# Optimization experiments

Hardware: AMD Instinct MI355X
Metric: run time of the kernel (lower is better)

Reference implementation:

```python
import jax, jax.numpy as jnp
import numpy as np
import math

D_MODEL = 2048
NUM_HEADS = 16
QUERY_GROUPS = 4
HEAD_DIM = D_MODEL // NUM_HEADS  # 128
B, T = 2, 2048


def setup_inputs() -> dict:
    key = jax.random.key(0)
    ks = jax.random.split(key, 9)
    s = 0.02
    return {
        "x": jax.random.normal(ks[0], (B, T, D_MODEL), dtype=jnp.float32),
        "Wq": jax.random.normal(ks[1], (D_MODEL, NUM_HEADS * HEAD_DIM), dtype=jnp.float32) * s,
        "bq": jnp.zeros((NUM_HEADS * HEAD_DIM,), dtype=jnp.float32),
        "Wk": jax.random.normal(ks[2], (D_MODEL, QUERY_GROUPS * HEAD_DIM), dtype=jnp.float32) * s,
        "bk": jnp.zeros((QUERY_GROUPS * HEAD_DIM,), dtype=jnp.float32),
        "Wv": jax.random.normal(ks[3], (D_MODEL, QUERY_GROUPS * HEAD_DIM), dtype=jnp.float32) * s,
        "bv": jnp.zeros((QUERY_GROUPS * HEAD_DIM,), dtype=jnp.float32),
        "Wo": jax.random.normal(ks[4], (D_MODEL, D_MODEL), dtype=jnp.float32) * s,
        "bo": jnp.zeros((D_MODEL,), dtype=jnp.float32),
    }


def reference(x, Wq, bq, Wk, bk, Wv, bv, Wo, bo):
    Bb, Tt, Dd = x.shape
    G, H, hd = QUERY_GROUPS, NUM_HEADS, HEAD_DIM
    m = H // G  # heads per group
    # projections
    q = (x @ Wq + bq).reshape(Bb, Tt, G, m, hd)   # [B,T,G,m,hd]
    k = (x @ Wk + bk).reshape(Bb, Tt, G, hd)      # [B,T,G,hd]
    v = (x @ Wv + bv).reshape(Bb, Tt, G, hd)
    # scores with native group broadcast (no explicit K/V expansion)
    scores = jnp.einsum('btgmd,bsgd->bgmts', q, k) / math.sqrt(hd)  # [B,G,m,T,T]
    p = jax.nn.softmax(scores, axis=-1)
    out = jnp.einsum('bgmts,bsgd->btgmd', p, v).reshape(Bb, Tt, Dd)
    # output projection (dropout is identity in eval / p=0)
    return out @ Wo + bo
```

## Files before the change

### kernel.cpp

```cpp
#include <hip/hip_runtime.h>

#define D_MODEL 2048
#define T_SEQ   2048
#define NBATCH  2
#define NH      16
#define NG      4
#define HD      128
#define NQKV    3072

typedef short bf16x8 __attribute__((ext_vector_type(8)));
typedef float f32x4  __attribute__((ext_vector_type(4)));
typedef short s16x4  __attribute__((ext_vector_type(4)));

__device__ __forceinline__ short f2bf(float f) {
  union { float f; unsigned u; } v; v.f = f;
  unsigned r = v.u + 0x7fffu + ((v.u >> 16) & 1u);
  return (short)(r >> 16);
}

__device__ __forceinline__ short f2bf_fast(float f) {
  union { float f; unsigned u; } v; v.f = f;
  return (short)((v.u + 0x8000u) >> 16);
}

__device__ __forceinline__ float bf2f(short s) {
  union { unsigned u; float f; } v; v.u = ((unsigned)(unsigned short)s) << 16;
  return v.f;
}

__device__ __forceinline__ float fast_exp2(float x) {
#if __has_builtin(__builtin_amdgcn_exp2f)
  return __builtin_amdgcn_exp2f(x);
#else
  return __expf(x * 0.6931471805599453f);
#endif
}

__device__ __forceinline__ void gload16(const void* g, void* l) {
  __builtin_amdgcn_global_load_lds(
      (const __attribute__((address_space(1))) void*)g,
      (__attribute__((address_space(3))) void*)l, 16, 0, 0);
}

__global__ __launch_bounds__(256) void convert_x_kernel(
    const float* __restrict__ x, short* __restrict__ o, int n) {
  int i = (blockIdx.x * 256 + threadIdx.x) * 4;
  if (i >= n) return;
  float4 v = *(const float4*)(x + i);
  s16x4 s;
  s[0] = f2bf(v.x); s[1] = f2bf(v.y); s[2] = f2bf(v.z); s[3] = f2bf(v.w);
  *(s16x4*)(o + i) = s;
}

__global__ __launch_bounds__(256) void wtrans_kernel(
    const float* __restrict__ W, short* __restrict__ dst,
    int K, int N, int rowOff, int dstStride) {
  __shared__ float t[32][33];
  int tx = threadIdx.x & 31, ty = threadIdx.x >> 5;
  int kb = blockIdx.x * 32, nb = blockIdx.y * 32;
#pragma unroll
  for (int i = 0; i < 4; ++i)
    t[ty + 8*i][tx] = W[(long)(kb + ty + 8*i) * N + nb + tx];
  __syncthreads();
#pragma unroll
  for (int i = 0; i < 4; ++i)
    dst[(long)(rowOff + nb + ty + 8*i) * dstStride + kb + tx] = f2bf(t[tx][ty + 8*i]);
}

__global__ __launch_bounds__(256) void vtrans_kernel(
    const short* __restrict__ qkv, short* __restrict__ vt) {
  __shared__ short t[32][33];
  int bg = blockIdx.z; int b = bg >> 2, g = bg & 3;
  int sb = blockIdx.x * 32, db = blockIdx.y * 32;
  int tx = threadIdx.x & 31, ty = threadIdx.x >> 5;
  const short* src = qkv + (long)(b * T_SEQ) * NQKV + D_MODEL + NG * HD + g * HD;
#pragma unroll
  for (int i = 0; i < 4; ++i)
    t[ty + 8*i][tx] = src[(long)(sb + ty + 8*i) * NQKV + db + tx];
  __syncthreads();
  short* dst = vt + ((long)bg * HD + db) * T_SEQ + sb;
#pragma unroll
  for (int i = 0; i < 4; ++i)
    dst[(long)(ty + 8*i) * T_SEQ + tx] = t[tx][ty + 8*i];
}

__global__ __launch_bounds__(256) void gemm_kernel(
    const short* __restrict__ A, const short* __restrict__ BT,
    const float* __restrict__ b0, const float* __restrict__ b1, const float* __restrict__ b2,
    void* __restrict__ Cout, int M, int N, int K, int mode) {
  __shared__ __align__(16) short As[128 * 64];
  __shared__ __align__(16) short Bs[128 * 64];
  const int tid = threadIdx.x;
  const int w = tid >> 6, lane = tid & 63;
  const int l15 = lane & 15, quad = lane >> 4;
  const int wr = w & 1, wc = w >> 1;
  const int nb = blockIdx.x, mb = blockIdx.y;
  const short* Ab = A + (long)mb * 128 * K;
  const short* Bb = BT + (long)nb * 128 * K;

  f32x4 acc[4][4];
#pragma unroll
  for (int i = 0; i < 4; ++i)
#pragma unroll
    for (int j = 0; j < 4; ++j) acc[i][j] = 0.0f;

  for (int k0 = 0; k0 < K; k0 += 64) {
    __syncthreads();
#pragma unroll
    for (int t = 0; t < 4; ++t) {
      int chunk = w * 256 + t * 64 + lane;
      int r = chunk >> 3, c = chunk & 7;
      int gc = c ^ (r & 7);
      gload16(Ab + (long)r * K + k0 + gc * 8, As + (w * 256 + t * 64) * 8);
      gload16(Bb + (long)r * K + k0 + gc * 8, Bs + (w * 256 + t * 64) * 8);
    }
    __syncthreads();
#pragma unroll
    for (int ks = 0; ks < 2; ++ks) {
      bf16x8 af[4], bfr[4];
#pragma unroll
      for (int i = 0; i < 4; ++i) {
        int r = wr * 64 + i * 16 + l15;
        af[i] = *(const bf16x8*)(As + r * 64 + (((ks * 4 + quad) ^ (r & 7)) * 8));
      }
#pragma unroll
      for (int j = 0; j < 4; ++j) {
        int r = wc * 64 + j * 16 + l15;
        bfr[j] = *(const bf16x8*)(Bs + r * 64 + (((ks * 4 + quad) ^ (r & 7)) * 8));
      }
#pragma unroll
      for (int i = 0; i < 4; ++i)
#pragma unroll
        for (int j = 0; j < 4; ++j)
          acc[i][j] = __builtin_amdgcn_mfma_f32_16x16x32_bf16(af[i], bfr[j], acc[i][j], 0, 0, 0);
    }
  }

  float biasv[4];
#pragma unroll
  for (int j = 0; j < 4; ++j) {
    int col = nb * 128 + wc * 64 + j * 16 + l15;
    float bv;
    if (mode == 0) {
      if (col < 2048)      bv = b0[col];
      else if (col < 2560) bv = b1[col - 2048];
      else                 bv = b2[col - 2560];
    } else bv = b0[col];
    biasv[j] = bv;
  }
  if (mode == 0) {
    short* C = (short*)Cout;
#pragma unroll
    for (int i = 0; i < 4; ++i)
#pragma unroll
      for (int j = 0; j < 4; ++j)
#pragma unroll
        for (int r = 0; r < 4; ++r) {
          int row = mb * 128 + wr * 64 + i * 16 + quad * 4 + r;
          int col = nb * 128 + wc * 64 + j * 16 + l15;
          C[(long)row * N + col] = f2bf(acc[i][j][r] + biasv[j]);
        }
  } else {
    float* C = (float*)Cout;
#pragma unroll
    for (int i = 0; i < 4; ++i)
#pragma unroll
      for (int j = 0; j < 4; ++j)
#pragma unroll
        for (int r = 0; r < 4; ++r) {
          int row = mb * 128 + wr * 64 + i * 16 + quad * 4 + r;
          int col = nb * 128 + wc * 64 + j * 16 + l15;
          C[(long)row * N + col] = acc[i][j][r] + biasv[j];
        }
  }
}

__global__ __launch_bounds__(256, 2) void attn_kernel(
    const short* __restrict__ qkv, const short* __restrict__ vt,
    short* __restrict__ aout) {
  __shared__ __align__(16) short smem[24576];
  short* Ks = smem;
  short* Vs = smem + 8192;
  short* Ps = smem + 16384;

  const int tid = threadIdx.x;
  const int w = tid >> 6, lane = tid & 63;
  const int l15 = lane & 15, quad = lane >> 4;
  const int qt = blockIdx.x, h = blockIdx.y, b = blockIdx.z;
  const int g = h >> 2;
  const short* qbase = qkv + (long)(b * T_SEQ + qt * 128) * NQKV + h * HD;
  const short* kbase = qkv + (long)(b * T_SEQ) * NQKV + D_MODEL + g * HD;
  const short* vbase = vt + (long)(b * NG + g) * HD * T_SEQ;
  const float QSCALE = 0.08838834764831845f * 1.4426950408889634f;

  int kroff[4], vroff[4], kdst[4], vdst[4];
#pragma unroll
  for (int t = 0; t < 4; ++t) {
    int chunk = w * 256 + t * 64 + lane;
    { int r = chunk >> 4, c = chunk & 15, gc = c ^ (r & 15);
      kroff[t] = r * NQKV + gc * 8; }
    { int r = chunk >> 3, c = chunk & 7, gc = c ^ (r & 7);
      vroff[t] = r * T_SEQ + gc * 8; }
    kdst[t] = chunk * 8; vdst[t] = chunk * 8;
  }

  bf16x8 qfrag[2][4];
#pragma unroll
  for (int set = 0; set < 2; ++set) {
    int qr = w * 32 + set * 16 + l15;
#pragma unroll
    for (int ks = 0; ks < 4; ++ks) {
      bf16x8 v = *(const bf16x8*)(qbase + (long)qr * NQKV + ks * 32 + quad * 8);
#pragma unroll
      for (int e = 0; e < 8; ++e) v[e] = f2bf(bf2f(v[e]) * QSCALE);
      qfrag[set][ks] = v;
    }
  }

#pragma unroll
  for (int t = 0; t < 4; ++t) {
    gload16(kbase + kroff[t], Ks + (w * 256 + t * 64) * 8);
    gload16(vbase + vroff[t], Vs + (w * 256 + t * 64) * 8);
  }

  bf16x8 ones;
#pragma unroll
  for (int e = 0; e < 8; ++e) ones[e] = (short)0x3F80;

  f32x4 lacc[2] = {f32x4(0.0f), f32x4(0.0f)};
  f32x4 oacc[2][8];
#pragma unroll
  for (int set = 0; set < 2; ++set)
#pragma unroll
    for (int j = 0; j < 8; ++j) oacc[set][j] = 0.0f;

  __syncthreads();

  bf16x8 kpre[4], vpre[4];
  for (int st = 0; st < T_SEQ / 64; ++st) {
    const bool pf = (st + 1 < T_SEQ / 64);
    if (pf) {
      const short* kb2 = kbase + (long)(st + 1) * 64 * NQKV;
      const short* vb2 = vbase + (st + 1) * 64;
#pragma unroll
      for (int t = 0; t < 4; ++t) {
        kpre[t] = *(const bf16x8*)(kb2 + kroff[t]);
        vpre[t] = *(const bf16x8*)(vb2 + vroff[t]);
      }
    }

    f32x4 sacc[2][4];
#pragma unroll
    for (int set = 0; set < 2; ++set)
#pragma unroll
      for (int j = 0; j < 4; ++j) sacc[set][j] = 0.0f;
    __builtin_amdgcn_s_setprio(1);
#pragma unroll
    for (int ks = 0; ks < 4; ++ks) {
#pragma unroll
      for (int j = 0; j < 4; ++j) {
        int krow = j * 16 + l15;
        bf16x8 bfr = *(const bf16x8*)(Ks + krow * 128 + (((ks * 4 + quad) ^ (krow & 15)) * 8));
        sacc[0][j] = __builtin_amdgcn_mfma_f32_16x16x32_bf16(qfrag[0][ks], bfr, sacc[0][j], 0, 0, 0);
        sacc[1][j] = __builtin_amdgcn_mfma_f32_16x16x32_bf16(qfrag[1][ks], bfr, sacc[1][j], 0, 0, 0);
      }
    }
    __builtin_amdgcn_s_setprio(0);

#pragma unroll
    for (int set = 0; set < 2; ++set)
#pragma unroll
      for (int j = 0; j < 4; ++j)
#pragma unroll
        for (int r = 0; r < 4; ++r) {
          short pb = f2bf_fast(fast_exp2(sacc[set][j][r]));
          int row = w * 32 + set * 16 + quad * 4 + r;
          int col = j * 16 + l15;
          Ps[row * 64 + (((col >> 3) ^ (row & 7)) * 8) + (col & 7)] = pb;
        }

    const int qr0 = w * 32 + l15, qr1 = qr0 + 16;
    __builtin_amdgcn_s_setprio(1);
#pragma unroll
    for (int ks = 0; ks < 2; ++ks) {
      bf16x8 af0 = *(const bf16x8*)(Ps + qr0 * 64 + (((ks * 4 + quad) ^ (qr0 & 7)) * 8));
      bf16x8 af1 = *(const bf16x8*)(Ps + qr1 * 64 + (((ks * 4 + quad) ^ (qr1 & 7)) * 8));
      lacc[0] = __builtin_amdgcn_mfma_f32_16x16x32_bf16(af0, ones, lacc[0], 0, 0, 0);
      lacc[1] = __builtin_amdgcn_mfma_f32_16x16x32_bf16(af1, ones, lacc[1], 0, 0, 0);
#pragma unroll
      for (int j = 0; j < 8; ++j) {
        int vrow = j * 16 + l15;
        bf16x8 bfr = *(const bf16x8*)(Vs + vrow * 64 + (((ks * 4 + quad) ^ (vrow & 7)) * 8));
        oacc[0][j] = __builtin_amdgcn_mfma_f32_16x16x32_bf16(af0, bfr, oacc[0][j], 0, 0, 0);
        oacc[1][j] = __builtin_amdgcn_mfma_f32_16x16x32_bf16(af1, bfr, oacc[1][j], 0, 0, 0);
      }
    }
    __builtin_amdgcn_s_setprio(0);

    __syncthreads();
    if (pf) {
#pragma unroll
      for (int t = 0; t < 4; ++t) {
        *(bf16x8*)(Ks + kdst[t]) = kpre[t];
        *(bf16x8*)(Vs + vdst[t]) = vpre[t];
      }
    }
    __syncthreads();
  }

  short* obase = aout + (long)(b * T_SEQ + qt * 128) * D_MODEL + h * HD;
#pragma unroll
  for (int set = 0; set < 2; ++set) {
    float inv[4];
#pragma unroll
    for (int r = 0; r < 4; ++r) inv[r] = 1.0f / lacc[set][r];
#pragma unroll
    for (int j = 0; j < 8; ++j)
#pragma unroll
      for (int r = 0; r < 4; ++r) {
        int row = w * 32 + set * 16 + quad * 4 + r;
        int col = j * 16 + l15;
        obase[(long)row * D_MODEL + col] = f2bf(oacc[set][j][r] * inv[r]);
      }
  }
}

extern "C" void kernel_launch(void* const* d_in, const int* in_sizes, int n_in,
                              void* d_out, int out_size, void* d_ws, size_t ws_size,
                              hipStream_t stream) {
  const float* x  = (const float*)d_in[0];
  const float* Wq = (const float*)d_in[1];
  const float* bq = (const float*)d_in[2];
  const float* Wk = (const float*)d_in[3];
  const float* bk = (const float*)d_in[4];
  const float* Wv = (const float*)d_in[5];
  const float* bv = (const float*)d_in[6];
  const float* Wo = (const float*)d_in[7];
  const float* bo = (const float*)d_in[8];

  const long NTOK = (long)NBATCH * T_SEQ;
  short* xb    = (short*)d_ws;
  short* wqkvT = xb + NTOK * D_MODEL;
  short* woT   = wqkvT + (long)NQKV * D_MODEL;
  short* qkvb  = woT + (long)D_MODEL * D_MODEL;
  short* vtb   = qkvb + NTOK * NQKV;
  short* attnb = vtb + (long)NBATCH * NG * HD * T_SEQ;

  int nX = (int)(NTOK * D_MODEL);
  convert_x_kernel<<<nX / (256 * 4), 256, 0, stream>>>(x, xb, nX);
  wtrans_kernel<<<dim3(D_MODEL / 32, D_MODEL / 32), 256, 0, stream>>>(Wq, wqkvT, D_MODEL, D_MODEL, 0, D_MODEL);
  wtrans_kernel<<<dim3(D_MODEL / 32, 512 / 32), 256, 0, stream>>>(Wk, wqkvT, D_MODEL, 512, 2048, D_MODEL);
  wtrans_kernel<<<dim3(D_MODEL / 32, 512 / 32), 256, 0, stream>>>(Wv, wqkvT, D_MODEL, 512, 2560, D_MODEL);
  wtrans_kernel<<<dim3(D_MODEL / 32, D_MODEL / 32), 256, 0, stream>>>(Wo, woT, D_MODEL, D_MODEL, 0, D_MODEL);

  gemm_kernel<<<dim3(NQKV / 128, NTOK / 128), 256, 0, stream>>>(
      xb, wqkvT, bq, bk, bv, (void*)qkvb, (int)NTOK, NQKV, D_MODEL, 0);

  vtrans_kernel<<<dim3(T_SEQ / 32, HD / 32, NBATCH * NG), 256, 0, stream>>>(qkvb, vtb);

  attn_kernel<<<dim3(T_SEQ / 128, NH, NBATCH), 256, 0, stream>>>(qkvb, vtb, attnb);

  gemm_kernel<<<dim3(D_MODEL / 128, NTOK / 128), 256, 0, stream>>>(
      attnb, woT, bo, bo, bo, (void*)d_out, (int)NTOK, D_MODEL, D_MODEL, 1);
}
```

Baseline: 330.9 us.

## Compute transposed attention with 32x32 MFMA, keep P in registers, stage output via LDS

Rewrites the attention inner loop to compute S^T = K·Q^T with 32x32x16 MFMAs, so each lane holds a query column's scores. The exponentiated scores are packed to bf16 with v_cvt_pk_bf16 and exchanged across half-waves with shuffles to form the P operand directly, removing the LDS round-trip for P and its extra LDS buffer. The row sum is accumulated in registers instead of via an MFMA against ones, and the output is staged through LDS so it can be written as coalesced 16-byte stores. The trade-off is more cross-lane shuffle and select work per tile and a higher register demand from the 16-wide accumulators.

```diff
diff --git a/kernel.cpp b/kernel.cpp
--- a/kernel.cpp
+++ b/kernel.cpp
@@ -10,17 +10,13 @@
 
 typedef short bf16x8 __attribute__((ext_vector_type(8)));
 typedef float f32x4  __attribute__((ext_vector_type(4)));
+typedef float f32x16 __attribute__((ext_vector_type(16)));
 typedef short s16x4  __attribute__((ext_vector_type(4)));
 
 __device__ __forceinline__ short f2bf(float f) {
   union { float f; unsigned u; } v; v.f = f;
   unsigned r = v.u + 0x7fffu + ((v.u >> 16) & 1u);
   return (short)(r >> 16);
-}
-
-__device__ __forceinline__ short f2bf_fast(float f) {
-  union { float f; unsigned u; } v; v.f = f;
-  return (short)((v.u + 0x8000u) >> 16);
 }
 
 __device__ __forceinline__ float bf2f(short s) {
@@ -34,6 +30,12 @@
 #else
   return __expf(x * 0.6931471805599453f);
 #endif
+}
+
+__device__ __forceinline__ unsigned cvt_pk_bf16(float a, float b) {
+  unsigned r;
+  asm("v_cvt_pk_bf16_f32 %0, %1, %2" : "=v"(r) : "v"(a), "v"(b));
+  return r;
 }
 
 __device__ __forceinline__ void gload16(const void* g, void* l) {
@@ -178,14 +180,13 @@
 __global__ __launch_bounds__(256, 2) void attn_kernel(
     const short* __restrict__ qkv, const short* __restrict__ vt,
     short* __restrict__ aout) {
-  __shared__ __align__(16) short smem[24576];
+  __shared__ __align__(16) short smem[16384];
   short* Ks = smem;
   short* Vs = smem + 8192;
-  short* Ps = smem + 16384;
 
   const int tid = threadIdx.x;
   const int w = tid >> 6, lane = tid & 63;
-  const int l15 = lane & 15, quad = lane >> 4;
+  const int l31 = lane & 31, hi = lane >> 5;
   const int qt = blockIdx.x, h = blockIdx.y, b = blockIdx.z;
   const int g = h >> 2;
   const short* qbase = qkv + (long)(b * T_SEQ + qt * 128) * NQKV + h * HD;
@@ -193,7 +194,7 @@
   const short* vbase = vt + (long)(b * NG + g) * HD * T_SEQ;
   const float QSCALE = 0.08838834764831845f * 1.4426950408889634f;
 
-  int kroff[4], vroff[4], kdst[4], vdst[4];
+  int kroff[4], vroff[4], dst[4];
 #pragma unroll
   for (int t = 0; t < 4; ++t) {
     int chunk = w * 256 + t * 64 + lane;
@@ -201,38 +202,31 @@
       kroff[t] = r * NQKV + gc * 8; }
     { int r = chunk >> 3, c = chunk & 7, gc = c ^ (r & 7);
       vroff[t] = r * T_SEQ + gc * 8; }
-    kdst[t] = chunk * 8; vdst[t] = chunk * 8;
-  }
-
-  bf16x8 qfrag[2][4];
-#pragma unroll
-  for (int set = 0; set < 2; ++set) {
-    int qr = w * 32 + set * 16 + l15;
-#pragma unroll
-    for (int ks = 0; ks < 4; ++ks) {
-      bf16x8 v = *(const bf16x8*)(qbase + (long)qr * NQKV + ks * 32 + quad * 8);
+    dst[t] = chunk * 8;
+  }
+
+  bf16x8 qfrag[8];
+  {
+    const short* qrow = qbase + (long)(w * 32 + l31) * NQKV + hi * 8;
+#pragma unroll
+    for (int ks = 0; ks < 8; ++ks) {
+      bf16x8 v = *(const bf16x8*)(qrow + ks * 16);
 #pragma unroll
       for (int e = 0; e < 8; ++e) v[e] = f2bf(bf2f(v[e]) * QSCALE);
-      qfrag[set][ks] = v;
+      qfrag[ks] = v;
     }
   }
 
 #pragma unroll
   for (int t = 0; t < 4; ++t) {
-    gload16(kbase + kroff[t], Ks + (w * 256 + t * 64) * 8);
-    gload16(vbase + vroff[t], Vs + (w * 256 + t * 64) * 8);
-  }
-
-  bf16x8 ones;
-#pragma unroll
-  for (int e = 0; e < 8; ++e) ones[e] = (short)0x3F80;
-
-  f32x4 lacc[2] = {f32x4(0.0f), f32x4(0.0f)};
-  f32x4 oacc[2][8];
-#pragma unroll
-  for (int set = 0; set < 2; ++set)
-#pragma unroll
-    for (int j = 0; j < 8; ++j) oacc[set][j] = 0.0f;
+    gload16(kbase + kroff[t], Ks + dst[t]);
+    gload16(vbase + vroff[t], Vs + dst[t]);
+  }
+
+  f32x16 oaccT[4];
+#pragma unroll
+  for (int i = 0; i < 4; ++i) oaccT[i] = 0.0f;
+  float lpart[4] = {0.f, 0.f, 0.f, 0.f};
 
   __syncthreads();
 
@@ -249,50 +243,52 @@
       }
     }
 
-    f32x4 sacc[2][4];
-#pragma unroll
-    for (int set = 0; set < 2; ++set)
-#pragma unroll
-      for (int j = 0; j < 4; ++j) sacc[set][j] = 0.0f;
+    f32x16 sacc[2];
+    sacc[0] = 0.0f; sacc[1] = 0.0f;
     __builtin_amdgcn_s_setprio(1);
 #pragma unroll
-    for (int ks = 0; ks < 4; ++ks) {
-#pragma unroll
-      for (int j = 0; j < 4; ++j) {
-        int krow = j * 16 + l15;
-        bf16x8 bfr = *(const bf16x8*)(Ks + krow * 128 + (((ks * 4 + quad) ^ (krow & 15)) * 8));
-        sacc[0][j] = __builtin_amdgcn_mfma_f32_16x16x32_bf16(qfrag[0][ks], bfr, sacc[0][j], 0, 0, 0);
-        sacc[1][j] = __builtin_amdgcn_mfma_f32_16x16x32_bf16(qfrag[1][ks], bfr, sacc[1][j], 0, 0, 0);
+    for (int ks = 0; ks < 8; ++ks) {
+#pragma unroll
+      for (int sb = 0; sb < 2; ++sb) {
+        int srow = sb * 32 + l31;
+        bf16x8 a = *(const bf16x8*)(Ks + srow * 128 + (((ks * 2 + hi) ^ (srow & 15)) * 8));
+        sacc[sb] = __builtin_amdgcn_mfma_f32_32x32x16_bf16(a, qfrag[ks], sacc[sb], 0, 0, 0);
       }
     }
     __builtin_amdgcn_s_setprio(0);
 
-#pragma unroll
-    for (int set = 0; set < 2; ++set)
-#pragma unroll
-      for (int j = 0; j < 4; ++j)
-#pragma unroll
-        for (int r = 0; r < 4; ++r) {
-          short pb = f2bf_fast(fast_exp2(sacc[set][j][r]));
-          int row = w * 32 + set * 16 + quad * 4 + r;
-          int col = j * 16 + l15;
-          Ps[row * 64 + (((col >> 3) ^ (row & 7)) * 8) + (col & 7)] = pb;
-        }
-
-    const int qr0 = w * 32 + l15, qr1 = qr0 + 16;
+    float p0[16], p1[16];
+#pragma unroll
+    for (int r = 0; r < 16; ++r) p0[r] = fast_exp2(sacc[0][r]);
+#pragma unroll
+    for (int r = 0; r < 16; ++r) p1[r] = fast_exp2(sacc[1][r]);
+#pragma unroll
+    for (int r = 0; r < 16; ++r) lpart[r & 3] += p0[r] + p1[r];
+
     __builtin_amdgcn_s_setprio(1);
 #pragma unroll
-    for (int ks = 0; ks < 2; ++ks) {
-      bf16x8 af0 = *(const bf16x8*)(Ps + qr0 * 64 + (((ks * 4 + quad) ^ (qr0 & 7)) * 8));
-      bf16x8 af1 = *(const bf16x8*)(Ps + qr1 * 64 + (((ks * 4 + quad) ^ (qr1 & 7)) * 8));
-      lacc[0] = __builtin_amdgcn_mfma_f32_16x16x32_bf16(af0, ones, lacc[0], 0, 0, 0);
-      lacc[1] = __builtin_amdgcn_mfma_f32_16x16x32_bf16(af1, ones, lacc[1], 0, 0, 0);
-#pragma unroll
-      for (int j = 0; j < 8; ++j) {
-        int vrow = j * 16 + l15;
-        bf16x8 bfr = *(const bf16x8*)(Vs + vrow * 64 + (((ks * 4 + quad) ^ (vrow & 7)) * 8));
-        oacc[0][j] = __builtin_amdgcn_mfma_f32_16x16x32_bf16(af0, bfr, oacc[0][j], 0, 0, 0);
-        oacc[1][j] = __builtin_amdgcn_mfma_f32_16x16x32_bf16(af1, bfr, oacc[1][j], 0, 0, 0);
+    for (int k2 = 0; k2 < 4; ++k2) {
+      const float* pp = (k2 & 2) ? p1 : p0;
+      const int bo = (k2 & 1) * 8;
+      unsigned Pa = cvt_pk_bf16(pp[bo + 0], pp[bo + 1]);
+      unsigned Pb = cvt_pk_bf16(pp[bo + 2], pp[bo + 3]);
+      unsigned Pc = cvt_pk_bf16(pp[bo + 4], pp[bo + 5]);
+      unsigned Pd = cvt_pk_bf16(pp[bo + 6], pp[bo + 7]);
+      unsigned ta = __shfl_xor(Pa, 32);
+      unsigned tb = __shfl_xor(Pb, 32);
+      unsigned tc = __shfl_xor(Pc, 32);
+      unsigned td = __shfl_xor(Pd, 32);
+      unsigned w0 = hi ? tc : Pa;
+      unsigned w1 = hi ? td : Pb;
+      unsigned w2 = hi ? Pc : ta;
+      unsigned w3 = hi ? Pd : tb;
+      union { unsigned u[4]; bf16x8 v; } pfr;
+      pfr.u[0] = w0; pfr.u[1] = w1; pfr.u[2] = w2; pfr.u[3] = w3;
+#pragma unroll
+      for (int db = 0; db < 4; ++db) {
+        int drow = db * 32 + l31;
+        bf16x8 a = *(const bf16x8*)(Vs + drow * 64 + (((k2 * 2 + hi) ^ (drow & 7)) * 8));
+        oaccT[db] = __builtin_amdgcn_mfma_f32_32x32x16_bf16(a, pfr.v, oaccT[db], 0, 0, 0);
       }
     }
     __builtin_amdgcn_s_setprio(0);
@@ -301,27 +297,37 @@
     if (pf) {
 #pragma unroll
       for (int t = 0; t < 4; ++t) {
-        *(bf16x8*)(Ks + kdst[t]) = kpre[t];
-        *(bf16x8*)(Vs + vdst[t]) = vpre[t];
+        *(bf16x8*)(Ks + dst[t]) = kpre[t];
+        *(bf16x8*)(Vs + dst[t]) = vpre[t];
       }
     }
     __syncthreads();
   }
 
+  float lsum = (lpart[0] + lpart[1]) + (lpart[2] + lpart[3]);
+  float lfull = lsum + __shfl_xor(lsum, 32);
+  float inv = 1.0f / lfull;
+
+  short* Osm = smem;
+  const int qrl = w * 32 + l31;
+#pragma unroll
+  for (int db = 0; db < 4; ++db)
+#pragma unroll
+    for (int r = 0; r < 16; ++r) {
+      int dloc = (r & 3) + 8 * (r >> 2) + 4 * hi;
+      int d = db * 32 + dloc;
+      int c = d >> 3;
+      Osm[qrl * 128 + ((c ^ (qrl & 15)) * 8) + (d & 7)] = f2bf(oaccT[db][r] * inv);
+    }
+  __syncthreads();
+
   short* obase = aout + (long)(b * T_SEQ + qt * 128) * D_MODEL + h * HD;
-#pragma unroll
-  for (int set = 0; set < 2; ++set) {
-    float inv[4];
-#pragma unroll
-    for (int r = 0; r < 4; ++r) inv[r] = 1.0f / lacc[set][r];
-#pragma unroll
-    for (int j = 0; j < 8; ++j)
-#pragma unroll
-      for (int r = 0; r < 4; ++r) {
-        int row = w * 32 + set * 16 + quad * 4 + r;
-        int col = j * 16 + l15;
-        obase[(long)row * D_MODEL + col] = f2bf(oacc[set][j][r] * inv[r]);
-      }
+  const int row = tid >> 1, ch = tid & 1;
+#pragma unroll
+  for (int j = 0; j < 8; ++j) {
+    int c2 = ch * 8 + j;
+    bf16x8 v = *(const bf16x8*)(Osm + row * 128 + ((c2 ^ (row & 15)) * 8));
+    *(bf16x8*)(obase + (long)row * D_MODEL + c2 * 8) = v;
   }
 }
 
```

New measurement: 335.9 us. About the same (+1.5%).
